# Kernel tuning notes

Hardware: AMD Instinct MI355X
Metric: run time of the kernel (lower is better)

Reference implementation:

```python
import jax, jax.numpy as jnp
import numpy as np

# ---- static dims ----
B, L, V = 8, 512, 100000
E, NERD, COREFD = 100, 20, 20          # word / ner / coref embedding dims
H, DIS, REL, HT = 128, 20, 97, 512     # hidden, dis embed, relations, n_pairs
W, N, R, C = 512, 32, 8, 256           # DNC word len, cells, read heads, ctrl hidden
IN_SIZE = E + NERD + COREFD            # 140 == H + 12 (required by final_layer)
DNC_OUT = H + 12                        # 140
CTRL_IN = IN_SIZE + R * W               # 4236
MASK_MIN, EPS, CLIP = 0.1, 1e-6, 20.0
# interface vector layout: read keys, read strengths, write key, write strength,
# erase, write vec, free gates, alloc gate, write gate, read modes,
# write mask, read masks, fwd sharpness, bwd sharpness
XI_SIZES = [R*W, R, W, 1, W, W, R, 1, 1, 3*R, W, R*W, R, R]
XI = sum(XI_SIZES)


def setup_inputs():
    key = jax.random.key(0)
    ks = iter(jax.random.split(key, 40))
    def nrm(shape, s=0.02):
        return (jax.random.normal(next(ks), shape) * s).astype(jnp.float32)
    def ri(shape, hi):
        return jax.random.randint(next(ks), shape, 0, hi)
    return dict(
        context_idxs=ri((B, L), V),
        pos=ri((B, L), L),
        context_ner=ri((B, L), 7),
        context_char_idxs=ri((B, L, 16), 262),
        context_lens=jnp.full((B,), L, dtype=jnp.int32),
        h_mapping=jax.random.uniform(next(ks), (B, HT, L), jnp.float32) / L,
        t_mapping=jax.random.uniform(next(ks), (B, HT, L), jnp.float32) / L,
        relation_mask=jnp.ones((B, HT), jnp.float32),
        dis_h_2_t=ri((B, HT), 20),
        dis_t_2_h=ri((B, HT), 20),
        word_emb=nrm((V, E), 0.1),
        entity_emb=nrm((L, COREFD), 0.1),
        ner_emb=nrm((7, NERD), 0.1),
        dis_emb=nrm((20, DIS), 0.1),
        Wih0=nrm((CTRL_IN, 4*C)), Whh0=nrm((C, 4*C)), b0=jnp.zeros((4*C,), jnp.float32),
        Wih1=nrm((C, 4*C)), Whh1=nrm((C, 4*C)), b1=jnp.zeros((4*C,), jnp.float32),
        Wih2=nrm((C, 4*C)), Whh2=nrm((C, 4*C)), b2=jnp.zeros((4*C,), jnp.float32),
        W_xi=nrm((C, XI)), b_xi=jnp.zeros((XI,), jnp.float32),
        W_out=nrm((C + R*W, DNC_OUT)), b_out=jnp.zeros((DNC_OUT,), jnp.float32),
        W_final=nrm((DNC_OUT, 2*H)), b_final=jnp.zeros((2*H,), jnp.float32),
        W_re=nrm((2*H, H)), b_re=jnp.zeros((H,), jnp.float32),
        W_bili=nrm((REL, H+DIS, H+DIS)), b_bili=jnp.zeros((REL,), jnp.float32),
    )


def _lstm(x, h, c, Wih, Whh, b):
    z = x @ Wih + h @ Whh + b
    i, f, g, o = jnp.split(z, 4, axis=-1)
    c = jax.nn.sigmoid(f) * c + jax.nn.sigmoid(i) * jnp.tanh(g)
    h = jax.nn.sigmoid(o) * jnp.tanh(c)
    return h, c


def _content(M, key_, beta, mask):
    # M [B,N,W]; key_, mask [B,h,W]; beta [B,h] -> weights [B,h,N]
    k = key_ * mask
    Mm = M[:, None] * mask[:, :, None]                 # [B,h,N,W]
    dot = jnp.einsum('bhw,bhnw->bhn', k, Mm)
    kn = jnp.linalg.norm(k, axis=-1)[..., None]
    Mn = jnp.linalg.norm(Mm, axis=-1)
    cos = dot / (kn * Mn + EPS)
    return jax.nn.softmax(beta[..., None] * cos, axis=-1)


def _sharpen(w, s):
    w = (w + EPS) ** s[..., None]
    return w / w.sum(-1, keepdims=True)


def _dnc(x, params):
    (Wih0, Whh0, b0, Wih1, Whh1, b1, Wih2, Whh2, b2, W_xi, b_xi, W_out, b_out) = params
    Bs = x.shape[0]
    eye = jnp.eye(N, dtype=x.dtype)
    splits = np.cumsum(XI_SIZES)[:-1]

    def step(carry, x_t):
        (h0, c0, h1, c1, h2, c2, M, u, wr, ww, p, Lnk, reads) = carry
        ci = jnp.concatenate([x_t, reads.reshape(Bs, R*W)], -1)
        h0, c0 = _lstm(ci, h0, c0, Wih0, Whh0, b0)
        h1, c1 = _lstm(h0, h1, c1, Wih1, Whh1, b1)
        h2, c2 = _lstm(h1, h2, c2, Wih2, Whh2, b2)
        h = jnp.clip(h2, -CLIP, CLIP)
        xi = h @ W_xi + b_xi
        (rk, rb, wk, wb, er, wv, fg, ga, gw, rm,
         wmask, rmask, sf, sb) = jnp.split(xi, splits, axis=-1)
        rk = rk.reshape(Bs, R, W)
        rb = 1 + jax.nn.softplus(rb)                    # [B,R]
        wk = wk.reshape(Bs, 1, W)
        wb = 1 + jax.nn.softplus(wb)                    # [B,1]
        er = jax.nn.sigmoid(er)                         # [B,W]
        fg = jax.nn.sigmoid(fg)                         # [B,R]
        ga = jax.nn.sigmoid(ga)
        gw = jax.nn.sigmoid(gw)
        pi = jax.nn.softmax(rm.reshape(Bs, R, 3), -1)
        wmask = MASK_MIN + (1 - MASK_MIN) * jax.nn.sigmoid(wmask)
        rmask = MASK_MIN + (1 - MASK_MIN) * jax.nn.sigmoid(rmask).reshape(Bs, R, W)
        sf = 1 + jax.nn.softplus(sf)
        sb = 1 + jax.nn.softplus(sb)

        # retention / usage
        psi = jnp.prod(1 - fg[:, :, None] * wr, axis=1)  # [B,N]
        u = (u + ww - u * ww) * psi
        # allocation weighting via sorted free list
        order = jnp.argsort(u, axis=-1)
        us = jnp.take_along_axis(u, order, -1)
        cp = jnp.cumprod(jnp.concatenate([jnp.ones((Bs, 1), u.dtype), us[:, :-1]], -1), -1)
        a_s = (1 - us) * cp
        a = jnp.zeros_like(u).at[jnp.arange(Bs)[:, None], order].set(a_s)
        # write addressing (masked content + allocation)
        cw = _content(M, wk, wb, wmask[:, None, :])[:, 0]
        ww = gw * (ga * a + (1 - ga) * cw)
        # de-allocate content of freed cells, then write
        M = M * psi[:, :, None]
        M = M * (1 - ww[:, :, None] * er[:, None, :]) + ww[:, :, None] * wv[:, None, :]
        # temporal link matrix (uses previous precedence p)
        Lnk = (1 - ww[:, :, None] - ww[:, None, :]) * Lnk + ww[:, :, None] * p[:, None, :]
        Lnk = Lnk * (1 - eye)
        p = (1 - ww.sum(-1, keepdims=True)) * p + ww
        # read addressing with link sharpness control
        fw = _sharpen(jnp.einsum('bij,brj->bri', Lnk, wr), sf)
        bw = _sharpen(jnp.einsum('bji,brj->bri', Lnk, wr), sb)
        cr = _content(M, rk, rb, rmask)
        wr = pi[..., 0:1] * bw + pi[..., 1:2] * cr + pi[..., 2:3] * fw
        reads = jnp.einsum('brn,bnw->brw', wr, M)
        y = jnp.concatenate([h, reads.reshape(Bs, R*W)], -1) @ W_out + b_out
        return (h0, c0, h1, c1, h2, c2, M, u, wr, ww, p, Lnk, reads), y

    z = jnp.zeros
    carry0 = (z((Bs, C)), z((Bs, C)), z((Bs, C)), z((Bs, C)), z((Bs, C)), z((Bs, C)),
              z((Bs, N, W)), z((Bs, N)), z((Bs, R, N)), z((Bs, N)), z((Bs, N)),
              z((Bs, N, N)), z((Bs, R, W)))
    _, ys = jax.lax.scan(step, carry0, x.transpose(1, 0, 2))
    return ys.transpose(1, 0, 2)  # [B,L,DNC_OUT]


def reference(context_idxs, pos, context_ner, context_char_idxs, context_lens,
              h_mapping, t_mapping, relation_mask, dis_h_2_t, dis_t_2_h,
              word_emb, entity_emb, ner_emb, dis_emb,
              Wih0, Whh0, b0, Wih1, Whh1, b1, Wih2, Whh2, b2,
              W_xi, b_xi, W_out, b_out, W_final, b_final, W_re, b_re,
              W_bili, b_bili):
    sent = jnp.concatenate([word_emb[context_idxs], entity_emb[pos],
                            ner_emb[context_ner]], -1)      # [B,L,140]
    dnc_params = (Wih0, Whh0, b0, Wih1, Whh1, b1, Wih2, Whh2, b2,
                  W_xi, b_xi, W_out, b_out)
    out = _dnc(sent, dnc_params)                             # [B,L,140]
    out = out @ W_final + b_final                            # LockedDropout: identity (eval)
    ctx = jax.nn.relu(out @ W_re + b_re)                     # [B,L,H]
    s0 = jnp.einsum('bpl,blh->bph', h_mapping, ctx)
    t0 = jnp.einsum('bpl,blh->bph', t_mapping, ctx)
    s_rep = jnp.concatenate([s0, dis_emb[dis_h_2_t]], -1)    # [B,P,148]
    t_rep = jnp.concatenate([t0, dis_emb[dis_t_2_h]], -1)
    return jnp.einsum('bpi,kij,bpj->bpk', s_rep, W_bili, t_rep) + b_bili
```

## Files before the change

kernel.cpp:

```cpp
#include <hip/hip_runtime.h>
#include <math.h>

#define B8      8
#define LSEQ    512
#define CDIM    256
#define GDIM    1024
#define WDIM    512
#define NCELL   32
#define RHEADS  8
#define XI_DIM  10299
#define DOUT    140
#define K_Z0    4492
#define K_Y     4352
#define HTP     512
#define RELK    97
#define BI      148

__device__ __forceinline__ float sigf(float x){
  return (x >= 0.f) ? 1.f/(1.f + expf(-x)) : expf(x)/(1.f + expf(x));
}
__device__ __forceinline__ float spf(float x){
  return (x > 0.f) ? x + log1pf(expf(-x)) : log1pf(expf(x));
}

__global__ __launch_bounds__(256)
void k_sent(const int* __restrict__ cidx, const int* __restrict__ pos,
            const int* __restrict__ ner, const float* __restrict__ wemb,
            const float* __restrict__ eemb, const float* __restrict__ nemb,
            float* __restrict__ sent)
{
  int flat = blockIdx.x*256 + threadIdx.x;
  if (flat >= B8*LSEQ*140) return;
  int d = flat % 140; int bl = flat / 140;
  float v;
  if (d < 100)      v = wemb[(size_t)cidx[bl]*100 + d];
  else if (d < 120) v = eemb[(size_t)pos[bl]*20 + (d-100)];
  else              v = nemb[(size_t)ner[bl]*20 + (d-120)];
  sent[flat] = v;
}

__global__ __launch_bounds__(256)
void k1_z0y(const float* __restrict__ Wih0, const float* __restrict__ Whh0,
            const float* __restrict__ b0,
            const float* __restrict__ Wout, const float* __restrict__ bout,
            const float* __restrict__ sent, const float* __restrict__ reads,
            const float* __restrict__ h0g, const float* __restrict__ Hh,
            float* __restrict__ z0, float* __restrict__ yh, int t, int yonly)
{
  __shared__ float sAin[B8][512];
  __shared__ float sRed[256][33];
  const int tid = threadIdx.x;
  const int wg  = blockIdx.x;
  const bool isY = (yonly != 0) || (wg >= 64);

  if (isY) {
    if (t == 0) return;
    const int yw = yonly ? wg : (wg - 64);
    const int c0 = yw*8;
    const int cq = tid & 1, ks = tid >> 1;
    float acc[8][4];
    for (int s=0;s<8;s++) for(int e=0;e<4;e++) acc[s][e]=0.f;
    const float* Hrow = Hh + (size_t)(t-1)*B8*CDIM;
    for (int kc = 0; kc < K_Y; kc += 512) {
      int klen = min(512, K_Y - kc);
      for (int ii=0; ii<16; ii++){
        int flat = tid + 256*ii; int s = flat >> 9; int kk = flat & 511;
        int g = kc + kk; float v = 0.f;
        if (kk < klen) v = (g < CDIM) ? Hrow[s*CDIM + g] : reads[s*4096 + (g-CDIM)];
        sAin[s][kk] = v;
      }
      __syncthreads();
      for (int k4=0; k4<4; k4++){
        int kk = ks*4 + k4;
        if (kk < klen) {
          int k = kc + kk;
          const float* wrow = Wout + (size_t)k*DOUT;
          float w[4];
          #pragma unroll
          for (int e=0;e<4;e++){ int c = c0 + cq*4 + e; w[e] = (c < DOUT) ? wrow[c] : 0.f; }
          #pragma unroll
          for (int s=0;s<8;s++){
            float a = sAin[s][kk];
            acc[s][0] += a*w[0]; acc[s][1] += a*w[1];
            acc[s][2] += a*w[2]; acc[s][3] += a*w[3];
          }
        }
      }
      __syncthreads();
    }
    for (int s=0;s<8;s++) for(int e=0;e<4;e++) sRed[tid][s*4+e] = acc[s][e];
    __syncthreads();
    if (tid < 64) {
      int cl = tid & 7, s = tid >> 3;
      int cq2 = (tid >> 2) & 1, ci = tid & 3;
      float sum = 0.f;
      for (int k2=0;k2<128;k2++) sum += sRed[cq2 + 2*k2][s*4+ci];
      int c = c0 + cl;
      if (c < DOUT) yh[((size_t)s*LSEQ + (t-1))*DOUT + c] = sum + bout[c];
    }
    return;
  }

  const int c0 = wg*16;
  const int cq = tid & 3, ks = tid >> 2;
  float acc[8][4];
  for (int s=0;s<8;s++) for(int e=0;e<4;e++) acc[s][e]=0.f;
  for (int kc = 0; kc < K_Z0; kc += 512) {
    int klen = min(512, K_Z0 - kc);
    for (int ii=0; ii<16; ii++){
      int flat = tid + 256*ii; int s = flat >> 9; int kk = flat & 511;
      int g = kc + kk; float v = 0.f;
      if (kk < klen) {
        if (g < 140)       v = sent[((size_t)s*LSEQ + t)*140 + g];
        else if (g < 4236) v = reads[s*4096 + (g-140)];
        else               v = h0g[s*CDIM + (g-4236)];
      }
      sAin[s][kk] = v;
    }
    __syncthreads();
    for (int k8=0; k8<8; k8++){
      int kk = ks*8 + k8;
      if (kk < klen) {
        int k = kc + kk;
        const float* wrow = (k < 4236) ? (Wih0 + (size_t)k*GDIM)
                                       : (Whh0 + (size_t)(k-4236)*GDIM);
        float4 w = *reinterpret_cast<const float4*>(wrow + c0 + cq*4);
        #pragma unroll
        for (int s=0;s<8;s++){
          float a = sAin[s][kk];
          acc[s][0] += a*w.x; acc[s][1] += a*w.y; acc[s][2] += a*w.z; acc[s][3] += a*w.w;
        }
      }
    }
    __syncthreads();
  }
  for (int s=0;s<8;s++) for(int e=0;e<4;e++) sRed[tid][s*4+e] = acc[s][e];
  __syncthreads();
  if (tid < 128) {
    int cl = tid & 15, s = tid >> 4;
    int cq2 = (tid >> 2) & 3, ci = tid & 3;
    float sum = 0.f;
    for (int k2=0;k2<64;k2++) sum += sRed[cq2 + 4*k2][s*4+ci];
    int c = c0 + cl;
    z0[s*GDIM + c] = sum + b0[c];
  }
}

__global__ __launch_bounds__(256)
void k_mid(const float* __restrict__ zin, float* __restrict__ cg, int par,
           float* __restrict__ houtg, const float* __restrict__ hsrc,
           const float* __restrict__ Wa, const float* __restrict__ Wb,
           const float* __restrict__ bias, float* __restrict__ zout)
{
  __shared__ float sAin[B8][512];
  __shared__ float sRed[256][33];
  const int tid = threadIdx.x, wg = blockIdx.x;
  for (int ii=0; ii<8; ii++){
    int cid = tid + 256*ii; int s = cid >> 8; int j = cid & 255;
    float zi = zin[s*GDIM + j],       zf = zin[s*GDIM + 256 + j];
    float zg = zin[s*GDIM + 512 + j], zo = zin[s*GDIM + 768 + j];
    float cold = cg[par*2048 + s*256 + j];
    float cn = sigf(zf)*cold + sigf(zi)*tanhf(zg);
    float h  = sigf(zo)*tanhf(cn);
    sAin[s][j] = h;
    if (wg == s) { cg[(par^1)*2048 + s*256 + j] = cn; houtg[s*256 + j] = h; }
  }
  for (int ii=0; ii<8; ii++){
    int cid = tid + 256*ii; int s = cid >> 8; int j = cid & 255;
    sAin[s][256 + j] = hsrc ? hsrc[s*256 + j] : 0.f;
  }
  __syncthreads();
  const int c0 = wg*16;
  const int cq = tid & 3, ks = tid >> 2;
  float acc[8][4];
  for (int s=0;s<8;s++) for(int e=0;e<4;e++) acc[s][e]=0.f;
  for (int k8=0;k8<8;k8++){
    int k = ks*8 + k8;
    const float* wrow = (k < 256) ? (Wa + (size_t)k*GDIM) : (Wb + (size_t)(k-256)*GDIM);
    float4 w = *reinterpret_cast<const float4*>(wrow + c0 + cq*4);
    #pragma unroll
    for (int s=0;s<8;s++){
      float a = sAin[s][k];
      acc[s][0] += a*w.x; acc[s][1] += a*w.y; acc[s][2] += a*w.z; acc[s][3] += a*w.w;
    }
  }
  for (int s=0;s<8;s++) for(int e=0;e<4;e++) sRed[tid][s*4+e] = acc[s][e];
  __syncthreads();
  if (tid < 128) {
    int cl = tid & 15, s = tid >> 4;
    int cq2 = (tid >> 2) & 3, ci = tid & 3;
    float sum = 0.f;
    for (int k2=0;k2<64;k2++) sum += sRed[cq2 + 4*k2][s*4+ci];
    int c = c0 + cl;
    zout[s*GDIM + c] = sum + bias[c];
  }
}

__global__ __launch_bounds__(256)
void k4_xi(const float* __restrict__ z2, float* __restrict__ c2g, int par,
           float* __restrict__ Hh, const float* __restrict__ Wxi,
           const float* __restrict__ bxi, float* __restrict__ xi, int t)
{
  __shared__ float sH[B8][CDIM];
  __shared__ float sRed[256][33];
  const int tid = threadIdx.x, wg = blockIdx.x;
  for (int ii=0; ii<8; ii++){
    int cid = tid + 256*ii; int s = cid >> 8; int j = cid & 255;
    float zi = z2[s*GDIM + j],       zf = z2[s*GDIM + 256 + j];
    float zg = z2[s*GDIM + 512 + j], zo = z2[s*GDIM + 768 + j];
    float cold = c2g[par*2048 + s*256 + j];
    float cn = sigf(zf)*cold + sigf(zi)*tanhf(zg);
    float h  = sigf(zo)*tanhf(cn);
    h = fminf(fmaxf(h, -20.f), 20.f);
    sH[s][j] = h;
    if (wg == s) { c2g[(par^1)*2048 + s*256 + j] = cn; Hh[((size_t)t*B8 + s)*CDIM + j] = h; }
  }
  __syncthreads();
  const int c0 = wg*64;
  const int cq = tid & 15, ks = tid >> 4;
  float acc[8][4];
  for (int s=0;s<8;s++) for(int e=0;e<4;e++) acc[s][e]=0.f;
  for (int k16=0;k16<16;k16++){
    int k = ks*16 + k16;
    const float* wrow = Wxi + (size_t)k*XI_DIM;
    float w[4];
    #pragma unroll
    for (int e=0;e<4;e++){ int c = c0 + cq*4 + e; w[e] = (c < XI_DIM) ? wrow[c] : 0.f; }
    #pragma unroll
    for (int s=0;s<8;s++){
      float a = sH[s][k];
      acc[s][0] += a*w[0]; acc[s][1] += a*w[1]; acc[s][2] += a*w[2]; acc[s][3] += a*w[3];
    }
  }
  for (int s=0;s<8;s++) for(int e=0;e<4;e++) sRed[tid][s*4+e] = acc[s][e];
  __syncthreads();
  for (int o = tid; o < 512; o += 256){
    int cq2 = (o >> 2) & 15, ci = o & 3, s = o >> 6;
    float sum = 0.f;
    for (int k2=0;k2<16;k2++) sum += sRed[cq2 + 16*k2][s*4+ci];
    int c = c0 + (o & 63);
    if (c < XI_DIM) xi[(size_t)s*XI_DIM + c] = sum + bxi[c];
  }
}

__global__ __launch_bounds__(512)
void k5_mem(const float* __restrict__ xi_g, float* __restrict__ M_g,
            float* __restrict__ u_g, float* __restrict__ ww_g, float* __restrict__ p_g,
            float* __restrict__ wr_g, float* __restrict__ L_g,
            float* __restrict__ reads_g)
{
  const int s = blockIdx.x;
  const int tid = threadIdx.x;
  const float* xi = xi_g + (size_t)s*XI_DIM;
  float* M = M_g + (size_t)s*NCELL*WDIM;

  __shared__ float s_rk[RHEADS][WDIM], s_rm[RHEADS][WDIM];
  __shared__ float s_wk[WDIM], s_wm[WDIM], s_er[WDIM], s_wv[WDIM];
  __shared__ float s_L[NCELL][NCELL];
  __shared__ float s_wr[RHEADS][NCELL], s_wrn[RHEADS][NCELL], s_cr[RHEADS][NCELL];
  __shared__ float s_fw[RHEADS][NCELL], s_bw[RHEADS][NCELL];
  __shared__ float s_psi[NCELL], s_u[NCELL], s_us[NCELL], s_a[NCELL], s_cw[NCELL];
  __shared__ float s_wwn[NCELL], s_wwo[NCELL], s_p[NCELL];
  __shared__ int   s_ord[NCELL];
  __shared__ float s_rb[RHEADS], s_sf[RHEADS], s_sb[RHEADS], s_fg[RHEADS], s_kn[RHEADS];
  __shared__ float s_pi[RHEADS][3];
  __shared__ float s_sc[64];

  for (int ii=0; ii<8; ii++){
    int f = tid + 512*ii; int r = f >> 9, w = f & 511;
    s_rk[r][w] = xi[f];
    s_rm[r][w] = 0.1f + 0.9f*sigf(xi[6187 + f]);
  }
  s_wk[tid] = xi[4104 + tid];
  s_er[tid] = sigf(xi[4617 + tid]);
  s_wv[tid] = xi[5129 + tid];
  s_wm[tid] = 0.1f + 0.9f*sigf(xi[5675 + tid]);
  if (tid < RHEADS){
    s_rb[tid] = 1.f + spf(xi[4096 + tid]);
    s_fg[tid] = sigf(xi[5641 + tid]);
    s_sf[tid] = 1.f + spf(xi[10283 + tid]);
    s_sb[tid] = 1.f + spf(xi[10291 + tid]);
    float e0 = xi[5651+3*tid], e1 = xi[5651+3*tid+1], e2 = xi[5651+3*tid+2];
    float mx = fmaxf(e0, fmaxf(e1, e2));
    float x0 = expf(e0-mx), x1 = expf(e1-mx), x2 = expf(e2-mx);
    float inv = 1.f/(x0+x1+x2);
    s_pi[tid][0]=x0*inv; s_pi[tid][1]=x1*inv; s_pi[tid][2]=x2*inv;
  }
  if (tid == 0){
    s_sc[0] = 1.f + spf(xi[4616]);
    s_sc[1] = sigf(xi[5649]);
    s_sc[2] = sigf(xi[5650]);
  }
  if (tid < NCELL){
    s_u[tid]   = u_g[s*NCELL + tid];
    s_wwo[tid] = ww_g[s*NCELL + tid];
    s_p[tid]   = p_g[s*NCELL + tid];
  }
  if (tid < 256) s_wr[tid>>5][tid&31] = wr_g[s*256 + tid];
  for (int ii=0; ii<2; ii++){ int f = tid + 512*ii; s_L[f>>5][f&31] = L_g[s*1024 + f]; }
  __syncthreads();

  if (tid < NCELL){
    float psi = 1.f;
    #pragma unroll
    for (int r=0;r<8;r++) psi *= (1.f - s_fg[r]*s_wr[r][tid]);
    s_psi[tid] = psi;
    float uo = s_u[tid], wo = s_wwo[tid];
    s_u[tid] = (uo + wo - uo*wo)*psi;
  }
  __syncthreads();

  if (tid < NCELL){
    float un = s_u[tid]; int rank = 0;
    for (int m=0;m<NCELL;m++){
      float um = s_u[m];
      rank += (um < un) || (um == un && m < tid);
    }
    s_ord[rank] = tid;
  }
  __syncthreads();
  if (tid < NCELL) s_us[tid] = s_u[s_ord[tid]];
  __syncthreads();
  if (tid == 0){
    float cp = 1.f;
    for (int j=0;j<NCELL;j++){ s_a[s_ord[j]] = (1.f - s_us[j])*cp; cp *= s_us[j]; }
  }
  __syncthreads();

  {
    float v = s_wk[tid]*s_wm[tid];
    float q = v*v;
    for (int o=32;o;o>>=1) q += __shfl_down(q, o, 64);
    if ((tid & 63) == 0) s_sc[8 + (tid >> 6)] = q;
  }
  __syncthreads();
  if (tid == 0){ float q=0; for(int i=0;i<8;i++) q += s_sc[8+i]; s_sc[3] = sqrtf(q); }
  __syncthreads();
  {
    int n = tid >> 4, wsub = tid & 15;
    float d=0.f, q=0.f;
    for (int i=0;i<32;i++){
      int w = wsub + 16*i;
      float m = M[(size_t)n*WDIM + w]; float wm = s_wm[w];
      d += s_wk[w]*wm*wm*m; float t2 = m*wm; q += t2*t2;
    }
    for (int o=8;o;o>>=1){ d += __shfl_down(d,o,16); q += __shfl_down(q,o,16); }
    if (wsub == 0){
      float cs = d/(s_sc[3]*sqrtf(q) + 1e-6f);
      s_cw[n] = s_sc[0]*cs;
    }
  }
  __syncthreads();
  if (tid == 0){ float mx=-1e30f; for(int n=0;n<32;n++) mx = fmaxf(mx, s_cw[n]); s_sc[4]=mx; }
  __syncthreads();
  if (tid < NCELL) s_cw[tid] = expf(s_cw[tid] - s_sc[4]);
  __syncthreads();
  if (tid == 0){ float sm=0; for(int n=0;n<32;n++) sm += s_cw[n]; s_sc[5] = 1.f/sm; }
  __syncthreads();
  if (tid < NCELL) s_cw[tid] *= s_sc[5];
  __syncthreads();

  if (tid < NCELL) s_wwn[tid] = s_sc[2]*( s_sc[1]*s_a[tid] + (1.f - s_sc[1])*s_cw[tid] );
  __syncthreads();

  for (int ii=0; ii<32; ii++){
    int f = tid + 512*ii; int n = f >> 9, w = f & 511;
    size_t idx = (size_t)n*WDIM + w;
    float m = M[idx];
    m = m*s_psi[n]*(1.f - s_wwn[n]*s_er[w]) + s_wwn[n]*s_wv[w];
    M[idx] = m;
  }
  __syncthreads();

  for (int ii=0; ii<2; ii++){
    int f = tid + 512*ii; int i = f >> 5, j = f & 31;
    float nl = (1.f - s_wwn[i] - s_wwn[j])*s_L[i][j] + s_wwn[i]*s_p[j];
    s_L[i][j] = (i == j) ? 0.f : nl;
  }
  __syncthreads();
  if (tid == 0){ float sw=0; for(int n=0;n<32;n++) sw += s_wwn[n]; s_sc[6]=sw; }
  __syncthreads();
  if (tid < NCELL) s_p[tid] = (1.f - s_sc[6])*s_p[tid] + s_wwn[tid];
  __syncthreads();

  {
    int r = (tid >> 5) & 7, i = tid & 31; bool isB = (tid >= 256);
    float accv = 0.f;
    if (!isB){ for (int j=0;j<32;j++) accv += s_L[i][j]*s_wr[r][j]; }
    else     { for (int j=0;j<32;j++) accv += s_L[j][i]*s_wr[r][j]; }
    float sp = isB ? s_sb[r] : s_sf[r];
    float e = expf(sp*logf(accv + 1e-6f));
    if (!isB) s_fw[r][i] = e; else s_bw[r][i] = e;
  }
  __syncthreads();
  if (tid < 16){
    int r = tid & 7; float sm = 0.f;
    if (tid < 8){ for (int n=0;n<32;n++) sm += s_fw[r][n]; s_sc[16+r] = 1.f/sm; }
    else        { for (int n=0;n<32;n++) sm += s_bw[r][n]; s_sc[24+r] = 1.f/sm; }
  }
  __syncthreads();
  {
    int r = (tid >> 5) & 7, i = tid & 31; bool isB = (tid >= 256);
    if (!isB) s_fw[r][i] *= s_sc[16+r]; else s_bw[r][i] *= s_sc[24+r];
  }
  __syncthreads();

  {
    int r = tid >> 6, wsub = tid & 63;
    float q = 0.f;
    for (int i2=0;i2<8;i2++){ int w = wsub + 64*i2; float v = s_rk[r][w]*s_rm[r][w]; q += v*v; }
    for (int o=32;o;o>>=1) q += __shfl_down(q, o, 64);
    if (wsub == 0) s_kn[r] = sqrtf(q);
  }
  __syncthreads();
  {
    int r = tid >> 6, rem = tid & 63, n = rem >> 1, h = rem & 1;
    float d=0.f, q=0.f;
    for (int i2=0;i2<256;i2++){
      int w = h*256 + i2;
      float m = M[(size_t)n*WDIM + w]; float rm = s_rm[r][w];
      d += s_rk[r][w]*rm*rm*m; float t2 = m*rm; q += t2*t2;
    }
    d += __shfl_down(d,1,2); q += __shfl_down(q,1,2);
    if (h == 0){
      float cs = d/(s_kn[r]*sqrtf(q) + 1e-6f);
      s_cr[r][n] = s_rb[r]*cs;
    }
  }
  __syncthreads();
  if (tid < 8){
    int r = tid; float mx = -1e30f;
    for (int n=0;n<32;n++) mx = fmaxf(mx, s_cr[r][n]);
    float sm = 0.f;
    for (int n=0;n<32;n++){ float e = expf(s_cr[r][n]-mx); s_cr[r][n] = e; sm += e; }
    float inv = 1.f/sm;
    for (int n=0;n<32;n++) s_cr[r][n] *= inv;
  }
  __syncthreads();

  if (tid < 256){
    int r = tid >> 5, n = tid & 31;
    float v = s_pi[r][0]*s_bw[r][n] + s_pi[r][1]*s_cr[r][n] + s_pi[r][2]*s_fw[r][n];
    s_wrn[r][n] = v; wr_g[s*256 + tid] = v;
  }
  __syncthreads();

  {
    int r = tid >> 6, wsub = tid & 63;
    for (int i2=0;i2<8;i2++){
      int w = wsub + 64*i2;
      float accv = 0.f;
      for (int n=0;n<32;n++) accv += s_wrn[r][n]*M[(size_t)n*WDIM + w];
      reads_g[s*4096 + r*512 + w] = accv;
    }
  }
  if (tid < NCELL){
    u_g[s*NCELL + tid] = s_u[tid];
    ww_g[s*NCELL + tid] = s_wwn[tid];
    p_g[s*NCELL + tid] = s_p[tid];
  }
  for (int ii=0; ii<2; ii++){ int f = tid + 512*ii; L_g[s*1024 + f] = s_L[f>>5][f&31]; }
}

__global__ __launch_bounds__(256)
void gemm16(int M, int N, int K,
            const float* __restrict__ A, long long sAb, int lda,
            const float* __restrict__ Bm, long long sBb, int ldb,
            float* __restrict__ C, long long sCb, int ldc,
            const float* __restrict__ bias, int relu)
{
  __shared__ float sA[16*512];
  const int tid = threadIdx.x;
  const float* Ab = A + (size_t)blockIdx.y*sAb;
  const float* Bb = Bm + (size_t)blockIdx.y*sBb;
  float* Cb = C + (size_t)blockIdx.y*sCb;
  const int m0 = blockIdx.x*16;
  const int tot = 16*K;
  for (int f = tid; f < tot; f += 256) sA[f] = Ab[(size_t)m0*lda + f];
  __syncthreads();
  int c = (tid & 63)*4; int rg = tid >> 6;
  if (c >= N) return;
  float acc[4][4] = {};
  for (int k=0;k<K;k++){
    float4 bv = *reinterpret_cast<const float4*>(Bb + (size_t)k*ldb + c);
    #pragma unroll
    for (int rr=0;rr<4;rr++){
      float a = sA[(rg*4+rr)*K + k];
      acc[rr][0] += a*bv.x; acc[rr][1] += a*bv.y; acc[rr][2] += a*bv.z; acc[rr][3] += a*bv.w;
    }
  }
  for (int rr=0;rr<4;rr++){
    int m = m0 + rg*4 + rr;
    #pragma unroll
    for (int e=0;e<4;e++){
      float v = acc[rr][e] + (bias ? bias[c+e] : 0.f);
      if (relu) v = fmaxf(v, 0.f);
      Cb[(size_t)m*ldc + c + e] = v;
    }
  }
}

__global__ __launch_bounds__(256)
void bilin(const float* __restrict__ s0, const float* __restrict__ t0,
           const float* __restrict__ dis_emb, const int* __restrict__ dht,
           const int* __restrict__ dth, const float* __restrict__ Wb,
           const float* __restrict__ bb, float* __restrict__ out)
{
  __shared__ float sS[BI][33];
  __shared__ float sT[32][152];
  const int tid = threadIdx.x;
  const int bp0 = blockIdx.x*32;
  for (int f = tid; f < 32*BI; f += 256){
    int pp = f / BI, i = f % BI;
    int bp = bp0 + pp;
    float sv, tv;
    if (i < 128){ sv = s0[(size_t)bp*128 + i]; tv = t0[(size_t)bp*128 + i]; }
    else {
      sv = dis_emb[(size_t)dht[bp]*20 + (i-128)];
      tv = dis_emb[(size_t)dth[bp]*20 + (i-128)];
    }
    sS[i][pp] = sv; sT[pp][i] = tv;
  }
  __syncthreads();
  const int ppg = tid >> 5, jb = tid & 31;
  const int pp0 = ppg*4;
  const int k0 = blockIdx.y*49, kend = min(k0+49, RELK);
  for (int k = k0; k < kend; k++){
    const float* Wk = Wb + (size_t)k*BI*BI;
    float acc[4][5];
    #pragma unroll
    for (int a=0;a<4;a++) for (int b=0;b<5;b++) acc[a][b]=0.f;
    for (int i=0;i<BI;i++){
      float sv0 = sS[i][pp0], sv1 = sS[i][pp0+1], sv2 = sS[i][pp0+2], sv3 = sS[i][pp0+3];
      const float* wrow = Wk + i*BI;
      #pragma unroll
      for (int jj=0;jj<5;jj++){
        int j = jb + 32*jj;
        if (j < BI){
          float w = wrow[j];
          acc[0][jj] += sv0*w; acc[1][jj] += sv1*w; acc[2][jj] += sv2*w; acc[3][jj] += sv3*w;
        }
      }
    }
    float dot[4] = {0.f,0.f,0.f,0.f};
    #pragma unroll
    for (int jj=0;jj<5;jj++){
      int j = jb + 32*jj;
      if (j < BI){
        #pragma unroll
        for (int p4=0;p4<4;p4++) dot[p4] += acc[p4][jj]*sT[pp0+p4][j];
      }
    }
    #pragma unroll
    for (int p4=0;p4<4;p4++)
      for (int o=16;o;o>>=1) dot[p4] += __shfl_down(dot[p4], o, 32);
    if (jb == 0){
      #pragma unroll
      for (int p4=0;p4<4;p4++)
        out[(size_t)(bp0+pp0+p4)*RELK + k] = dot[p4] + bb[k];
    }
  }
}

extern "C" void kernel_launch(void* const* d_in, const int* in_sizes, int n_in,
                              void* d_out, int out_size, void* d_ws, size_t ws_size,
                              hipStream_t stream)
{
  (void)in_sizes; (void)n_in; (void)out_size; (void)ws_size;
  const int*   ctx_idx = (const int*)  d_in[0];
  const int*   pos     = (const int*)  d_in[1];
  const int*   nerI    = (const int*)  d_in[2];
  const float* h_map   = (const float*)d_in[5];
  const float* t_map   = (const float*)d_in[6];
  const int*   dht     = (const int*)  d_in[8];
  const int*   dth     = (const int*)  d_in[9];
  const float* wemb    = (const float*)d_in[10];
  const float* eemb    = (const float*)d_in[11];
  const float* nemb    = (const float*)d_in[12];
  const float* demb    = (const float*)d_in[13];
  const float* Wih0    = (const float*)d_in[14];
  const float* Whh0    = (const float*)d_in[15];
  const float* b0      = (const float*)d_in[16];
  const float* Wih1    = (const float*)d_in[17];
  const float* Whh1    = (const float*)d_in[18];
  const float* b1      = (const float*)d_in[19];
  const float* Wih2    = (const float*)d_in[20];
  const float* Whh2    = (const float*)d_in[21];
  const float* b2      = (const float*)d_in[22];
  const float* Wxi     = (const float*)d_in[23];
  const float* bxi     = (const float*)d_in[24];
  const float* Wout    = (const float*)d_in[25];
  const float* bout    = (const float*)d_in[26];
  const float* Wfin    = (const float*)d_in[27];
  const float* bfin    = (const float*)d_in[28];
  const float* Wre     = (const float*)d_in[29];
  const float* bre     = (const float*)d_in[30];
  const float* Wbili   = (const float*)d_in[31];
  const float* bbili   = (const float*)d_in[32];

  float* ws   = (float*)d_ws;
  float* sent = ws;
  float* Hh   = sent + 573440;
  float* yh   = Hh + 1048576;
  float* o256 = yh + 573440;
  float* ctxb = o256 + 1048576;
  float* s0b  = ctxb + 524288;
  float* t0b  = s0b + 524288;
  float* stateBase = t0b + 524288;
  float* reads = stateBase;
  float* h0g   = reads + 32768;
  float* h1g   = h0g + 2048;
  float* c0g   = h1g + 2048;
  float* c1g   = c0g + 4096;
  float* c2g   = c1g + 4096;
  float* z0    = c2g + 4096;
  float* z1    = z0 + 8192;
  float* z2    = z1 + 8192;
  float* xib   = z2 + 8192;
  float* Mb    = xib + 82392;
  float* ug    = Mb + 131072;
  float* wwg   = ug + 256;
  float* pg    = wwg + 256;
  float* wrg   = pg + 256;
  float* Lg    = wrg + 2048;
  float* stateEnd = Lg + 8192;
  size_t stateBytes = (size_t)(stateEnd - stateBase)*sizeof(float);
  hipMemsetAsync(stateBase, 0, stateBytes, stream);

  hipLaunchKernelGGL(k_sent, dim3((573440+255)/256), dim3(256), 0, stream,
                     ctx_idx, pos, nerI, wemb, eemb, nemb, sent);

  for (int t = 0; t < LSEQ; t++){
    int par = t & 1;
    hipLaunchKernelGGL(k1_z0y, dim3(82), dim3(256), 0, stream,
                       Wih0, Whh0, b0, Wout, bout, sent, reads, h0g, Hh, z0, yh, t, 0);
    hipLaunchKernelGGL(k_mid, dim3(64), dim3(256), 0, stream,
                       z0, c0g, par, h0g, h1g, Wih1, Whh1, b1, z1);
    hipLaunchKernelGGL(k_mid, dim3(64), dim3(256), 0, stream,
                       z1, c1g, par, h1g, (t > 0) ? (Hh + (size_t)(t-1)*2048) : (const float*)nullptr,
                       Wih2, Whh2, b2, z2);
    hipLaunchKernelGGL(k4_xi, dim3(161), dim3(256), 0, stream,
                       z2, c2g, par, Hh, Wxi, bxi, xib, t);
    hipLaunchKernelGGL(k5_mem, dim3(8), dim3(512), 0, stream,
                       xib, Mb, ug, wwg, pg, wrg, Lg, reads);
  }
  hipLaunchKernelGGL(k1_z0y, dim3(18), dim3(256), 0, stream,
                     Wih0, Whh0, b0, Wout, bout, sent, reads, h0g, Hh, z0, yh, LSEQ, 1);

  hipLaunchKernelGGL(gemm16, dim3(256,1), dim3(256), 0, stream,
                     4096, 256, 140, yh, (long long)0, 140, Wfin, (long long)0, 256,
                     o256, (long long)0, 256, bfin, 0);
  hipLaunchKernelGGL(gemm16, dim3(256,1), dim3(256), 0, stream,
                     4096, 128, 256, o256, (long long)0, 256, Wre, (long long)0, 128,
                     ctxb, (long long)0, 128, bre, 1);
  hipLaunchKernelGGL(gemm16, dim3(32,8), dim3(256), 0, stream,
                     512, 128, 512, h_map, (long long)(512*512), 512,
                     ctxb, (long long)(512*128), 128,
                     s0b, (long long)(512*128), 128, (const float*)nullptr, 0);
  hipLaunchKernelGGL(gemm16, dim3(32,8), dim3(256), 0, stream,
                     512, 128, 512, t_map, (long long)(512*512), 512,
                     ctxb, (long long)(512*128), 128,
                     t0b, (long long)(512*128), 128, (const float*)nullptr, 0);
  hipLaunchKernelGGL(bilin, dim3(128,2), dim3(256), 0, stream,
                     s0b, t0b, demb, dht, dth, Wbili, bbili, (float*)d_out);
}
```

Before: 80.88 ms.

## Replace per-timestep kernel launches with a persistent DNC kernel using grid barriers

Replaces the 2560 per-step kernel launches of the DNC recurrence with one persistent kernel of 256 workgroups that loops over all timesteps, separated by atomic grid-wide barriers. Each workgroup keeps its slice of the LSTM, interface and output weights resident in registers instead of reloading them from global memory every step. The memory-update phase is folded into the same kernel, and reads and hidden state are double-buffered to avoid races. The cost is heavy register pressure, a spin-barrier that depends on all 256 workgroups being co-resident, and more serialized per-step work.

```diff
diff --git a/kernel.cpp b/kernel.cpp
--- a/kernel.cpp
+++ b/kernel.cpp
@@ -3,16 +3,8 @@
 
 #define B8      8
 #define LSEQ    512
-#define CDIM    256
-#define GDIM    1024
-#define WDIM    512
-#define NCELL   32
-#define RHEADS  8
-#define XI_DIM  10299
-#define DOUT    140
-#define K_Z0    4492
-#define K_Y     4352
-#define HTP     512
+#define NWG     256
+#define TPB     512
 #define RELK    97
 #define BI      148
 
@@ -39,427 +31,492 @@
   sent[flat] = v;
 }
 
-__global__ __launch_bounds__(256)
-void k1_z0y(const float* __restrict__ Wih0, const float* __restrict__ Whh0,
-            const float* __restrict__ b0,
-            const float* __restrict__ Wout, const float* __restrict__ bout,
-            const float* __restrict__ sent, const float* __restrict__ reads,
-            const float* __restrict__ h0g, const float* __restrict__ Hh,
-            float* __restrict__ z0, float* __restrict__ yh, int t, int yonly)
+__device__ __forceinline__ void gbar(int* cnt, int* gen){
+  __syncthreads();
+  if (threadIdx.x == 0){
+    __threadfence();
+    int g = __hip_atomic_load(gen, __ATOMIC_RELAXED, __HIP_MEMORY_SCOPE_AGENT);
+    int v = __hip_atomic_fetch_add(cnt, 1, __ATOMIC_ACQ_REL, __HIP_MEMORY_SCOPE_AGENT);
+    if (v == NWG-1){
+      __hip_atomic_store(cnt, 0, __ATOMIC_RELAXED, __HIP_MEMORY_SCOPE_AGENT);
+      __hip_atomic_fetch_add(gen, 1, __ATOMIC_RELEASE, __HIP_MEMORY_SCOPE_AGENT);
+    } else {
+      while (__hip_atomic_load(gen, __ATOMIC_RELAXED, __HIP_MEMORY_SCOPE_AGENT) == g)
+        __builtin_amdgcn_s_sleep(1);
+    }
+    __threadfence();
+  }
+  __syncthreads();
+}
+
+__device__ void mem_phase(float* lds, const float* __restrict__ xi,
+                          float* __restrict__ M, float* u_g, float* ww_g,
+                          float* p_g, float* wr_g, float* L_g, float* rout)
 {
-  __shared__ float sAin[B8][512];
-  __shared__ float sRed[256][33];
   const int tid = threadIdx.x;
+  float* mL  = lds;
+  float* mwr = lds+1024;
+  float* mwrn= lds+1280;
+  float* mcr = lds+1536;
+  float* mfw = lds+1792;
+  float* mbw = lds+2048;
+  float* PSI = lds+2304;
+  float* UU  = lds+2336;
+  float* US  = lds+2368;
+  float* AA  = lds+2400;
+  float* CW  = lds+2432;
+  float* WWN = lds+2464;
+  float* WWO = lds+2496;
+  float* PP  = lds+2528;
+  int*   mord= (int*)(lds+2560);
+  float* mh  = lds+2592;
+  float* mpi = lds+2656;
+  float* msc = lds+2688;
+  float* mq1 = lds+2752;
+  float* mq2 = lds+3264;
+  float* mp1 = lds+3776;
+  float* mp2 = lds+4800;
+
+  if (tid < 8){
+    mh[tid]    = 1.f + spf(xi[4096+tid]);
+    mh[8+tid]  = 1.f + spf(xi[10283+tid]);
+    mh[16+tid] = 1.f + spf(xi[10291+tid]);
+    mh[24+tid] = sigf(xi[5641+tid]);
+    float e0=xi[5651+3*tid], e1=xi[5652+3*tid], e2=xi[5653+3*tid];
+    float mx=fmaxf(e0,fmaxf(e1,e2));
+    float x0=expf(e0-mx), x1=expf(e1-mx), x2=expf(e2-mx);
+    float inv=1.f/(x0+x1+x2);
+    mpi[tid*3]=x0*inv; mpi[tid*3+1]=x1*inv; mpi[tid*3+2]=x2*inv;
+  }
+  if (tid==0){ msc[0]=1.f+spf(xi[4616]); msc[1]=sigf(xi[5649]); msc[2]=sigf(xi[5650]); }
+  if (tid<32){ UU[tid]=u_g[tid]; WWO[tid]=ww_g[tid]; PP[tid]=p_g[tid]; }
+  if (tid<256) mwr[tid]=wr_g[tid];
+  mL[tid]=L_g[tid]; mL[tid+512]=L_g[tid+512];
+  { float wm = 0.1f+0.9f*sigf(xi[5675+tid]); mq1[tid]=xi[4104+tid]*wm; mq2[tid]=wm; }
+  __syncthreads();
+
+  if (tid<32){
+    float psi=1.f;
+    #pragma unroll
+    for (int r=0;r<8;r++) psi *= (1.f - mh[24+r]*mwr[r*32+tid]);
+    PSI[tid]=psi;
+    float uo=UU[tid], wo=WWO[tid];
+    UU[tid]=(uo+wo-uo*wo)*psi;
+  }
+  __syncthreads();
+  if (tid<32){
+    float un=UU[tid]; int rank=0;
+    for (int m=0;m<32;m++){ float um=UU[m]; rank += (um<un)||(um==un && m<tid); }
+    mord[rank]=tid;
+  }
+  __syncthreads();
+  if (tid<32) US[tid]=UU[mord[tid]];
+  __syncthreads();
+  if (tid==0){ float cp=1.f; for (int j=0;j<32;j++){ AA[mord[j]]=(1.f-US[j])*cp; cp*=US[j]; } }
+  __syncthreads();
+
+  { float q=mq1[tid]*mq1[tid];
+    for (int o=32;o;o>>=1) q += __shfl_down(q,o,64);
+    if ((tid&63)==0) msc[8+(tid>>6)]=q; }
+  __syncthreads();
+  if (tid==0){ float q=0.f; for (int i=0;i<8;i++) q+=msc[8+i]; msc[3]=sqrtf(q); }
+  __syncthreads();
+  { int n=tid>>4, wsub=tid&15;
+    float d=0.f,q=0.f;
+    for (int i=0;i<32;i++){ int w=wsub+16*i; float m=M[(size_t)n*512+w]; float t2=m*mq2[w]; d+=mq1[w]*t2; q+=t2*t2; }
+    for (int o=8;o;o>>=1){ d+=__shfl_down(d,o,16); q+=__shfl_down(q,o,16); }
+    if (wsub==0){ float cs=d/(msc[3]*sqrtf(q)+1e-6f); CW[n]=msc[0]*cs; } }
+  __syncthreads();
+  if (tid==0){ float mx=-1e30f; for(int n=0;n<32;n++) mx=fmaxf(mx,CW[n]); msc[4]=mx; }
+  __syncthreads();
+  if (tid<32) CW[tid]=expf(CW[tid]-msc[4]);
+  __syncthreads();
+  if (tid==0){ float sm=0.f; for(int n=0;n<32;n++) sm+=CW[n]; msc[5]=1.f/sm; }
+  __syncthreads();
+  if (tid<32) CW[tid]*=msc[5];
+  __syncthreads();
+  if (tid<32) WWN[tid]=msc[2]*(msc[1]*AA[tid]+(1.f-msc[1])*CW[tid]);
+  __syncthreads();
+  { float er=sigf(xi[4617+tid]); float wv=xi[5129+tid];
+    for (int n=0;n<32;n++){ size_t idx=(size_t)n*512+tid; float m=M[idx];
+      M[idx]=m*PSI[n]*(1.f-WWN[n]*er)+WWN[n]*wv; } }
+  __syncthreads();
+  for (int ii=0;ii<2;ii++){ int f=tid+512*ii; int i=f>>5, j=f&31;
+    float nl=(1.f-WWN[i]-WWN[j])*mL[f]+WWN[i]*PP[j];
+    mL[f]=(i==j)?0.f:nl; }
+  __syncthreads();
+  if (tid==0){ float sw=0.f; for(int n=0;n<32;n++) sw+=WWN[n]; msc[6]=sw; }
+  __syncthreads();
+  if (tid<32) PP[tid]=(1.f-msc[6])*PP[tid]+WWN[tid];
+  __syncthreads();
+  { int r=(tid>>5)&7, i=tid&31; bool isB=(tid>=256);
+    float accv=0.f;
+    if (!isB){ for (int j=0;j<32;j++) accv += mL[i*32+j]*mwr[r*32+j]; }
+    else     { for (int j=0;j<32;j++) accv += mL[j*32+i]*mwr[r*32+j]; }
+    float sp = isB? mh[16+r] : mh[8+r];
+    float e = expf(sp*logf(accv+1e-6f));
+    if (!isB) mfw[r*32+i]=e; else mbw[r*32+i]=e; }
+  __syncthreads();
+  if (tid<16){ int r=tid&7; float sm=0.f;
+    if (tid<8){ for(int n=0;n<32;n++) sm+=mfw[r*32+n]; msc[16+r]=1.f/sm; }
+    else      { for(int n=0;n<32;n++) sm+=mbw[r*32+n]; msc[24+r]=1.f/sm; } }
+  __syncthreads();
+  { int r=(tid>>5)&7, i=tid&31; bool isB=(tid>=256);
+    if (!isB) mfw[r*32+i]*=msc[16+r]; else mbw[r*32+i]*=msc[24+r]; }
+  __syncthreads();
+  for (int hp=0; hp<4; hp++){
+    for (int rp2=0;rp2<2;rp2++){
+      int r=hp*2+rp2;
+      float rm=0.1f+0.9f*sigf(xi[6187+r*512+tid]);
+      mp1[rp2*512+tid]=xi[r*512+tid]*rm;
+      mp2[rp2*512+tid]=rm;
+    }
+    __syncthreads();
+    for (int rp2=0;rp2<2;rp2++){
+      float q=mp1[rp2*512+tid]; q*=q;
+      for (int o=32;o;o>>=1) q+=__shfl_down(q,o,64);
+      if ((tid&63)==0) msc[8+(tid>>6)]=q;
+      __syncthreads();
+      if (tid==0){ float qq=0.f; for(int i=0;i<8;i++) qq+=msc[8+i]; msc[32+rp2]=sqrtf(qq); }
+      __syncthreads();
+    }
+    { int rp2=tid>>8, rem=tid&255, n=rem>>3, wsub=rem&7;
+      float d=0.f,q=0.f;
+      for (int i=0;i<64;i++){ int w=wsub*64+i; float m=M[(size_t)n*512+w]; float t2=m*mp2[rp2*512+w];
+        d+=mp1[rp2*512+w]*t2; q+=t2*t2; }
+      for (int o=4;o;o>>=1){ d+=__shfl_down(d,o,8); q+=__shfl_down(q,o,8); }
+      if (wsub==0){ int r=hp*2+rp2; float cs=d/(msc[32+rp2]*sqrtf(q)+1e-6f); mcr[r*32+n]=mh[r]*cs; } }
+    __syncthreads();
+  }
+  if (tid<8){ int r=tid; float mx=-1e30f;
+    for (int n=0;n<32;n++) mx=fmaxf(mx,mcr[r*32+n]);
+    float sm=0.f;
+    for (int n=0;n<32;n++){ float e=expf(mcr[r*32+n]-mx); mcr[r*32+n]=e; sm+=e; }
+    float inv=1.f/sm;
+    for (int n=0;n<32;n++) mcr[r*32+n]*=inv; }
+  __syncthreads();
+  if (tid<256){ int r=tid>>5, n=tid&31;
+    float v=mpi[r*3]*mbw[r*32+n]+mpi[r*3+1]*mcr[r*32+n]+mpi[r*3+2]*mfw[r*32+n];
+    mwrn[tid]=v; wr_g[tid]=v; }
+  __syncthreads();
+  { int r=tid>>6, wsub=tid&63;
+    for (int i2=0;i2<8;i2++){ int w=wsub+64*i2;
+      float accv=0.f;
+      for (int n=0;n<32;n++) accv+=mwrn[r*32+n]*M[(size_t)n*512+w];
+      rout[r*512+w]=accv; } }
+  if (tid<32){ u_g[tid]=UU[tid]; ww_g[tid]=WWN[tid]; p_g[tid]=PP[tid]; }
+  L_g[tid]=mL[tid]; L_g[tid+512]=mL[tid+512];
+}
+
+__global__ __launch_bounds__(TPB, 2)
+void dnc_persist(
+  const float* __restrict__ sent,
+  const float* __restrict__ Wih0, const float* __restrict__ Whh0, const float* __restrict__ b0,
+  const float* __restrict__ Wih1, const float* __restrict__ Whh1, const float* __restrict__ b1,
+  const float* __restrict__ Wih2, const float* __restrict__ Whh2, const float* __restrict__ b2,
+  const float* __restrict__ Wxi, const float* __restrict__ bxi,
+  const float* __restrict__ Wout, const float* __restrict__ bout,
+  float* __restrict__ Hh, float* __restrict__ yh,
+  float* __restrict__ reads2,
+  float* __restrict__ h0g, float* __restrict__ h1g, float* __restrict__ h2g,
+  float* __restrict__ c0g, float* __restrict__ c1g, float* __restrict__ c2g,
+  float* __restrict__ z0g, float* __restrict__ z1g, float* __restrict__ z2g,
+  float* __restrict__ xig,
+  float* __restrict__ Mb, float* __restrict__ ug, float* __restrict__ wwg,
+  float* __restrict__ pg, float* __restrict__ wrg, float* __restrict__ Lg,
+  int* bar)
+{
+  __shared__ float lds[5824];
+  float* sA   = lds;
+  float* sRed = lds + 4160;
   const int wg  = blockIdx.x;
-  const bool isY = (yonly != 0) || (wg >= 64);
-
-  if (isY) {
-    if (t == 0) return;
-    const int yw = yonly ? wg : (wg - 64);
-    const int c0 = yw*8;
-    const int cq = tid & 1, ks = tid >> 1;
-    float acc[8][4];
-    for (int s=0;s<8;s++) for(int e=0;e<4;e++) acc[s][e]=0.f;
-    const float* Hrow = Hh + (size_t)(t-1)*B8*CDIM;
-    for (int kc = 0; kc < K_Y; kc += 512) {
-      int klen = min(512, K_Y - kc);
-      for (int ii=0; ii<16; ii++){
-        int flat = tid + 256*ii; int s = flat >> 9; int kk = flat & 511;
-        int g = kc + kk; float v = 0.f;
-        if (kk < klen) v = (g < CDIM) ? Hrow[s*CDIM + g] : reads[s*4096 + (g-CDIM)];
-        sAin[s][kk] = v;
-      }
-      __syncthreads();
-      for (int k4=0; k4<4; k4++){
-        int kk = ks*4 + k4;
-        if (kk < klen) {
-          int k = kc + kk;
-          const float* wrow = Wout + (size_t)k*DOUT;
-          float w[4];
-          #pragma unroll
-          for (int e=0;e<4;e++){ int c = c0 + cq*4 + e; w[e] = (c < DOUT) ? wrow[c] : 0.f; }
+  const int tid = threadIdx.x;
+  const int cq = tid >> 7, kq = tid & 127;
+  const int xc = tid >> 6, xk = tid & 63;
+  int* cnt = bar; int* gen = bar+1;
+
+  const int zcol = wg*4 + cq;
+  float w0r[36];
+  #pragma unroll
+  for (int c=0;c<9;c++)
+    #pragma unroll
+    for (int i=0;i<4;i++){
+      int k = c*512 + kq*4 + i;
+      float v;
+      if (k < 4236)      v = Wih0[(size_t)k*1024 + zcol];
+      else if (k < 4492) v = Whh0[(size_t)(k-4236)*1024 + zcol];
+      else               v = 0.f;
+      w0r[c*4+i]=v;
+    }
+  float w1r[4], w2r[4];
+  #pragma unroll
+  for (int i=0;i<4;i++){
+    int k = kq*4+i;
+    w1r[i] = (k<256)? Wih1[(size_t)k*1024+zcol] : Whh1[(size_t)(k-256)*1024+zcol];
+    w2r[i] = (k<256)? Wih2[(size_t)k*1024+zcol] : Whh2[(size_t)(k-256)*1024+zcol];
+  }
+  float wxr[24];
+  #pragma unroll
+  for (int cc=0;cc<6;cc++){
+    int col = wg*48 + xc*6 + cc;
+    #pragma unroll
+    for (int i=0;i<4;i++){
+      int k = xk*4+i;
+      wxr[cc*4+i] = (col<10299)? Wxi[(size_t)k*10299 + col] : 0.f;
+    }
+  }
+  float wyr[9];
+  {
+    bool isy = (wg>=8 && wg<148);
+    int ycol = wg-8;
+    #pragma unroll
+    for (int c=0;c<9;c++){
+      int k = c*512 + tid;
+      wyr[c] = (isy && k<4352)? Wout[(size_t)k*140 + ycol] : 0.f;
+    }
+  }
+
+  #pragma unroll 1
+  for (int t=0; t<LSEQ; t++){
+    const int rp = t&1, wp = rp^1;
+    const float* readsPrev = reads2 + (size_t)((t-1)&1)*32768;
+
+    {
+      float acc[8] = {0,0,0,0,0,0,0,0};
+      const float* h0p = h0g + ((t-1)&1)*2048;
+      float av[8];
+      #pragma unroll
+      for (int s=0;s<8;s++){
+        int kg = tid;
+        float v;
+        if (kg < 140) v = sent[((size_t)s*512 + t)*140 + kg];
+        else          v = readsPrev[s*4096 + kg - 140];
+        av[s]=v;
+      }
+      for (int ch=0; ch<9; ch++){
+        __syncthreads();
+        #pragma unroll
+        for (int s=0;s<8;s++) sA[s*520 + tid] = av[s];
+        __syncthreads();
+        if (ch < 8){
+          int kg = (ch+1)*512 + tid;
           #pragma unroll
           for (int s=0;s<8;s++){
-            float a = sAin[s][kk];
-            acc[s][0] += a*w[0]; acc[s][1] += a*w[1];
-            acc[s][2] += a*w[2]; acc[s][3] += a*w[3];
+            float v;
+            if (kg < 140)       v = sent[((size_t)s*512 + t)*140 + kg];
+            else if (kg < 4236) v = readsPrev[s*4096 + kg - 140];
+            else if (kg < 4492) v = h0p[s*256 + (kg-4236)];
+            else                v = 0.f;
+            av[s]=v;
           }
         }
-      }
-      __syncthreads();
-    }
-    for (int s=0;s<8;s++) for(int e=0;e<4;e++) sRed[tid][s*4+e] = acc[s][e];
+        #pragma unroll
+        for (int s=0;s<8;s++){
+          float4 a = *reinterpret_cast<const float4*>(&sA[s*520 + (kq<<2)]);
+          acc[s] += a.x*w0r[ch*4] + a.y*w0r[ch*4+1] + a.z*w0r[ch*4+2] + a.w*w0r[ch*4+3];
+        }
+      }
+      #pragma unroll
+      for (int o=32;o;o>>=1)
+        #pragma unroll
+        for (int s=0;s<8;s++) acc[s]+=__shfl_down(acc[s],o,64);
+      if ((tid&63)==0){ int wv=tid>>6;
+        #pragma unroll
+        for (int s=0;s<8;s++) sRed[wv*8+s]=acc[s]; }
+      __syncthreads();
+      if (tid<32){ int c=tid>>3, s=tid&7;
+        z0g[s*1024 + wg*4 + c] = sRed[c*16+s] + sRed[c*16+8+s] + b0[wg*4+c]; }
+    }
+    gbar(cnt,gen);
+
+    {
+      if (tid<256){
+        int j=tid;
+        #pragma unroll
+        for (int s=0;s<8;s++){
+          float zi=z0g[s*1024+j], zf=z0g[s*1024+256+j], zg=z0g[s*1024+512+j], zo=z0g[s*1024+768+j];
+          float cold=c0g[rp*2048+s*256+j];
+          float cn=sigf(zf)*cold+sigf(zi)*tanhf(zg);
+          float h=sigf(zo)*tanhf(cn);
+          sA[s*520+j]=h;
+          if (wg==8){ c0g[wp*2048+s*256+j]=cn; h0g[rp*2048+s*256+j]=h; }
+        }
+      } else {
+        int j=tid-256;
+        const float* h1p = h1g + ((t-1)&1)*2048;
+        #pragma unroll
+        for (int s=0;s<8;s++) sA[s*520+256+j]=h1p[s*256+j];
+      }
+      __syncthreads();
+      float acc[8]={0,0,0,0,0,0,0,0};
+      #pragma unroll
+      for (int s=0;s<8;s++){
+        float4 a=*reinterpret_cast<const float4*>(&sA[s*520+(kq<<2)]);
+        acc[s]+=a.x*w1r[0]+a.y*w1r[1]+a.z*w1r[2]+a.w*w1r[3];
+      }
+      #pragma unroll
+      for (int o=32;o;o>>=1)
+        #pragma unroll
+        for (int s=0;s<8;s++) acc[s]+=__shfl_down(acc[s],o,64);
+      if ((tid&63)==0){ int wv=tid>>6;
+        #pragma unroll
+        for (int s=0;s<8;s++) sRed[wv*8+s]=acc[s]; }
+      __syncthreads();
+      if (tid<32){ int c=tid>>3, s=tid&7;
+        z1g[s*1024 + wg*4 + c] = sRed[c*16+s] + sRed[c*16+8+s] + b1[wg*4+c]; }
+    }
+    gbar(cnt,gen);
+
+    {
+      if (tid<256){
+        int j=tid;
+        #pragma unroll
+        for (int s=0;s<8;s++){
+          float zi=z1g[s*1024+j], zf=z1g[s*1024+256+j], zg=z1g[s*1024+512+j], zo=z1g[s*1024+768+j];
+          float cold=c1g[rp*2048+s*256+j];
+          float cn=sigf(zf)*cold+sigf(zi)*tanhf(zg);
+          float h=sigf(zo)*tanhf(cn);
+          sA[s*520+j]=h;
+          if (wg==8){ c1g[wp*2048+s*256+j]=cn; h1g[rp*2048+s*256+j]=h; }
+        }
+      } else {
+        int j=tid-256;
+        const float* h2p = h2g + ((t-1)&1)*2048;
+        #pragma unroll
+        for (int s=0;s<8;s++) sA[s*520+256+j]=h2p[s*256+j];
+      }
+      __syncthreads();
+      float acc[8]={0,0,0,0,0,0,0,0};
+      #pragma unroll
+      for (int s=0;s<8;s++){
+        float4 a=*reinterpret_cast<const float4*>(&sA[s*520+(kq<<2)]);
+        acc[s]+=a.x*w2r[0]+a.y*w2r[1]+a.z*w2r[2]+a.w*w2r[3];
+      }
+      #pragma unroll
+      for (int o=32;o;o>>=1)
+        #pragma unroll
+        for (int s=0;s<8;s++) acc[s]+=__shfl_down(acc[s],o,64);
+      if ((tid&63)==0){ int wv=tid>>6;
+        #pragma unroll
+        for (int s=0;s<8;s++) sRed[wv*8+s]=acc[s]; }
+      __syncthreads();
+      if (tid<32){ int c=tid>>3, s=tid&7;
+        z2g[s*1024 + wg*4 + c] = sRed[c*16+s] + sRed[c*16+8+s] + b2[wg*4+c]; }
+    }
+    gbar(cnt,gen);
+
+    {
+      if (tid<256){
+        int j=tid;
+        #pragma unroll
+        for (int s=0;s<8;s++){
+          float zi=z2g[s*1024+j], zf=z2g[s*1024+256+j], zg=z2g[s*1024+512+j], zo=z2g[s*1024+768+j];
+          float cold=c2g[rp*2048+s*256+j];
+          float cn=sigf(zf)*cold+sigf(zi)*tanhf(zg);
+          float h2=sigf(zo)*tanhf(cn);
+          float hc=fminf(fmaxf(h2,-20.f),20.f);
+          sA[s*520+j]=hc;
+          if (wg==8){ c2g[wp*2048+s*256+j]=cn; h2g[rp*2048+s*256+j]=h2;
+                      Hh[((size_t)t*8+s)*256+j]=hc; }
+        }
+      }
+      __syncthreads();
+      float accx[6][8];
+      #pragma unroll
+      for (int cc=0;cc<6;cc++)
+        #pragma unroll
+        for (int s=0;s<8;s++) accx[cc][s]=0.f;
+      #pragma unroll
+      for (int s=0;s<8;s++){
+        float4 a = *reinterpret_cast<const float4*>(&sA[s*520 + (xk<<2)]);
+        #pragma unroll
+        for (int cc=0;cc<6;cc++)
+          accx[cc][s] += a.x*wxr[cc*4] + a.y*wxr[cc*4+1] + a.z*wxr[cc*4+2] + a.w*wxr[cc*4+3];
+      }
+      #pragma unroll
+      for (int o=32;o;o>>=1)
+        #pragma unroll
+        for (int cc=0;cc<6;cc++)
+          #pragma unroll
+          for (int s=0;s<8;s++) accx[cc][s]+=__shfl_down(accx[cc][s],o,64);
+      if ((tid&63)==0){
+        #pragma unroll
+        for (int cc=0;cc<6;cc++){
+          int col = wg*48 + xc*6 + cc;
+          if (col < 10299){
+            #pragma unroll
+            for (int s=0;s<8;s++) xig[(size_t)s*10299+col]=accx[cc][s]+bxi[col];
+          }
+        }
+      }
+    }
+    gbar(cnt,gen);
+
+    if (wg < 8){
+      mem_phase(lds, xig + (size_t)wg*10299, Mb + (size_t)wg*16384,
+                ug+wg*32, wwg+wg*32, pg+wg*32, wrg+wg*256, Lg+wg*1024,
+                reads2 + (size_t)rp*32768 + wg*4096);
+    } else if (wg < 148 && t > 0){
+      int ty = t-1, col = wg-8;
+      const float* rdp = reads2 + (size_t)(ty&1)*32768;
+      float acy[8]={0,0,0,0,0,0,0,0};
+      #pragma unroll
+      for (int ch=0;ch<9;ch++){
+        int kg=ch*512+tid;
+        #pragma unroll
+        for (int s=0;s<8;s++){
+          float a;
+          if (kg<256)       a=Hh[((size_t)ty*8+s)*256+kg];
+          else if (kg<4352) a=rdp[s*4096+kg-256];
+          else              a=0.f;
+          acy[s]+=a*wyr[ch];
+        }
+      }
+      #pragma unroll
+      for (int o=32;o;o>>=1)
+        #pragma unroll
+        for (int s=0;s<8;s++) acy[s]+=__shfl_down(acy[s],o,64);
+      if ((tid&63)==0){ int wv=tid>>6;
+        #pragma unroll
+        for (int s=0;s<8;s++) sRed[wv*8+s]=acy[s]; }
+      __syncthreads();
+      if (tid<8){ float v=0.f;
+        #pragma unroll
+        for (int w=0;w<8;w++) v+=sRed[w*8+tid];
+        yh[((size_t)tid*512+ty)*140+col]=v+bout[col]; }
+    }
+    gbar(cnt,gen);
+  }
+
+  if (wg>=8 && wg<148){
+    int ty = 511, col = wg-8;
+    const float* rdp = reads2 + (size_t)(ty&1)*32768;
+    float acy[8]={0,0,0,0,0,0,0,0};
+    #pragma unroll
+    for (int ch=0;ch<9;ch++){
+      int kg=ch*512+tid;
+      #pragma unroll
+      for (int s=0;s<8;s++){
+        float a;
+        if (kg<256)       a=Hh[((size_t)ty*8+s)*256+kg];
+        else if (kg<4352) a=rdp[s*4096+kg-256];
+        else              a=0.f;
+        acy[s]+=a*wyr[ch];
+      }
+    }
+    #pragma unroll
+    for (int o=32;o;o>>=1)
+      #pragma unroll
+      for (int s=0;s<8;s++) acy[s]+=__shfl_down(acy[s],o,64);
+    if ((tid&63)==0){ int wv=tid>>6;
+      #pragma unroll
+      for (int s=0;s<8;s++) sRed[wv*8+s]=acy[s]; }
     __syncthreads();
-    if (tid < 64) {
-      int cl = tid & 7, s = tid >> 3;
-      int cq2 = (tid >> 2) & 1, ci = tid & 3;
-      float sum = 0.f;
-      for (int k2=0;k2<128;k2++) sum += sRed[cq2 + 2*k2][s*4+ci];
-      int c = c0 + cl;
-      if (c < DOUT) yh[((size_t)s*LSEQ + (t-1))*DOUT + c] = sum + bout[c];
-    }
-    return;
-  }
-
-  const int c0 = wg*16;
-  const int cq = tid & 3, ks = tid >> 2;
-  float acc[8][4];
-  for (int s=0;s<8;s++) for(int e=0;e<4;e++) acc[s][e]=0.f;
-  for (int kc = 0; kc < K_Z0; kc += 512) {
-    int klen = min(512, K_Z0 - kc);
-    for (int ii=0; ii<16; ii++){
-      int flat = tid + 256*ii; int s = flat >> 9; int kk = flat & 511;
-      int g = kc + kk; float v = 0.f;
-      if (kk < klen) {
-        if (g < 140)       v = sent[((size_t)s*LSEQ + t)*140 + g];
-        else if (g < 4236) v = reads[s*4096 + (g-140)];
-        else               v = h0g[s*CDIM + (g-4236)];
-      }
-      sAin[s][kk] = v;
-    }
-    __syncthreads();
-    for (int k8=0; k8<8; k8++){
-      int kk = ks*8 + k8;
-      if (kk < klen) {
-        int k = kc + kk;
-        const float* wrow = (k < 4236) ? (Wih0 + (size_t)k*GDIM)
-                                       : (Whh0 + (size_t)(k-4236)*GDIM);
-        float4 w = *reinterpret_cast<const float4*>(wrow + c0 + cq*4);
-        #pragma unroll
-        for (int s=0;s<8;s++){
-          float a = sAin[s][kk];
-          acc[s][0] += a*w.x; acc[s][1] += a*w.y; acc[s][2] += a*w.z; acc[s][3] += a*w.w;
-        }
-      }
-    }
-    __syncthreads();
-  }
-  for (int s=0;s<8;s++) for(int e=0;e<4;e++) sRed[tid][s*4+e] = acc[s][e];
-  __syncthreads();
-  if (tid < 128) {
-    int cl = tid & 15, s = tid >> 4;
-    int cq2 = (tid >> 2) & 3, ci = tid & 3;
-    float sum = 0.f;
-    for (int k2=0;k2<64;k2++) sum += sRed[cq2 + 4*k2][s*4+ci];
-    int c = c0 + cl;
-    z0[s*GDIM + c] = sum + b0[c];
-  }
-}
-
-__global__ __launch_bounds__(256)
-void k_mid(const float* __restrict__ zin, float* __restrict__ cg, int par,
-           float* __restrict__ houtg, const float* __restrict__ hsrc,
-           const float* __restrict__ Wa, const float* __restrict__ Wb,
-           const float* __restrict__ bias, float* __restrict__ zout)
-{
-  __shared__ float sAin[B8][512];
-  __shared__ float sRed[256][33];
-  const int tid = threadIdx.x, wg = blockIdx.x;
-  for (int ii=0; ii<8; ii++){
-    int cid = tid + 256*ii; int s = cid >> 8; int j = cid & 255;
-    float zi = zin[s*GDIM + j],       zf = zin[s*GDIM + 256 + j];
-    float zg = zin[s*GDIM + 512 + j], zo = zin[s*GDIM + 768 + j];
-    float cold = cg[par*2048 + s*256 + j];
-    float cn = sigf(zf)*cold + sigf(zi)*tanhf(zg);
-    float h  = sigf(zo)*tanhf(cn);
-    sAin[s][j] = h;
-    if (wg == s) { cg[(par^1)*2048 + s*256 + j] = cn; houtg[s*256 + j] = h; }
-  }
-  for (int ii=0; ii<8; ii++){
-    int cid = tid + 256*ii; int s = cid >> 8; int j = cid & 255;
-    sAin[s][256 + j] = hsrc ? hsrc[s*256 + j] : 0.f;
-  }
-  __syncthreads();
-  const int c0 = wg*16;
-  const int cq = tid & 3, ks = tid >> 2;
-  float acc[8][4];
-  for (int s=0;s<8;s++) for(int e=0;e<4;e++) acc[s][e]=0.f;
-  for (int k8=0;k8<8;k8++){
-    int k = ks*8 + k8;
-    const float* wrow = (k < 256) ? (Wa + (size_t)k*GDIM) : (Wb + (size_t)(k-256)*GDIM);
-    float4 w = *reinterpret_cast<const float4*>(wrow + c0 + cq*4);
-    #pragma unroll
-    for (int s=0;s<8;s++){
-      float a = sAin[s][k];
-      acc[s][0] += a*w.x; acc[s][1] += a*w.y; acc[s][2] += a*w.z; acc[s][3] += a*w.w;
-    }
-  }
-  for (int s=0;s<8;s++) for(int e=0;e<4;e++) sRed[tid][s*4+e] = acc[s][e];
-  __syncthreads();
-  if (tid < 128) {
-    int cl = tid & 15, s = tid >> 4;
-    int cq2 = (tid >> 2) & 3, ci = tid & 3;
-    float sum = 0.f;
-    for (int k2=0;k2<64;k2++) sum += sRed[cq2 + 4*k2][s*4+ci];
-    int c = c0 + cl;
-    zout[s*GDIM + c] = sum + bias[c];
-  }
-}
-
-__global__ __launch_bounds__(256)
-void k4_xi(const float* __restrict__ z2, float* __restrict__ c2g, int par,
-           float* __restrict__ Hh, const float* __restrict__ Wxi,
-           const float* __restrict__ bxi, float* __restrict__ xi, int t)
-{
-  __shared__ float sH[B8][CDIM];
-  __shared__ float sRed[256][33];
-  const int tid = threadIdx.x, wg = blockIdx.x;
-  for (int ii=0; ii<8; ii++){
-    int cid = tid + 256*ii; int s = cid >> 8; int j = cid & 255;
-    float zi = z2[s*GDIM + j],       zf = z2[s*GDIM + 256 + j];
-    float zg = z2[s*GDIM + 512 + j], zo = z2[s*GDIM + 768 + j];
-    float cold = c2g[par*2048 + s*256 + j];
-    float cn = sigf(zf)*cold + sigf(zi)*tanhf(zg);
-    float h  = sigf(zo)*tanhf(cn);
-    h = fminf(fmaxf(h, -20.f), 20.f);
-    sH[s][j] = h;
-    if (wg == s) { c2g[(par^1)*2048 + s*256 + j] = cn; Hh[((size_t)t*B8 + s)*CDIM + j] = h; }
-  }
-  __syncthreads();
-  const int c0 = wg*64;
-  const int cq = tid & 15, ks = tid >> 4;
-  float acc[8][4];
-  for (int s=0;s<8;s++) for(int e=0;e<4;e++) acc[s][e]=0.f;
-  for (int k16=0;k16<16;k16++){
-    int k = ks*16 + k16;
-    const float* wrow = Wxi + (size_t)k*XI_DIM;
-    float w[4];
-    #pragma unroll
-    for (int e=0;e<4;e++){ int c = c0 + cq*4 + e; w[e] = (c < XI_DIM) ? wrow[c] : 0.f; }
-    #pragma unroll
-    for (int s=0;s<8;s++){
-      float a = sH[s][k];
-      acc[s][0] += a*w[0]; acc[s][1] += a*w[1]; acc[s][2] += a*w[2]; acc[s][3] += a*w[3];
-    }
-  }
-  for (int s=0;s<8;s++) for(int e=0;e<4;e++) sRed[tid][s*4+e] = acc[s][e];
-  __syncthreads();
-  for (int o = tid; o < 512; o += 256){
-    int cq2 = (o >> 2) & 15, ci = o & 3, s = o >> 6;
-    float sum = 0.f;
-    for (int k2=0;k2<16;k2++) sum += sRed[cq2 + 16*k2][s*4+ci];
-    int c = c0 + (o & 63);
-    if (c < XI_DIM) xi[(size_t)s*XI_DIM + c] = sum + bxi[c];
-  }
-}
-
-__global__ __launch_bounds__(512)
-void k5_mem(const float* __restrict__ xi_g, float* __restrict__ M_g,
-            float* __restrict__ u_g, float* __restrict__ ww_g, float* __restrict__ p_g,
-            float* __restrict__ wr_g, float* __restrict__ L_g,
-            float* __restrict__ reads_g)
-{
-  const int s = blockIdx.x;
-  const int tid = threadIdx.x;
-  const float* xi = xi_g + (size_t)s*XI_DIM;
-  float* M = M_g + (size_t)s*NCELL*WDIM;
-
-  __shared__ float s_rk[RHEADS][WDIM], s_rm[RHEADS][WDIM];
-  __shared__ float s_wk[WDIM], s_wm[WDIM], s_er[WDIM], s_wv[WDIM];
-  __shared__ float s_L[NCELL][NCELL];
-  __shared__ float s_wr[RHEADS][NCELL], s_wrn[RHEADS][NCELL], s_cr[RHEADS][NCELL];
-  __shared__ float s_fw[RHEADS][NCELL], s_bw[RHEADS][NCELL];
-  __shared__ float s_psi[NCELL], s_u[NCELL], s_us[NCELL], s_a[NCELL], s_cw[NCELL];
-  __shared__ float s_wwn[NCELL], s_wwo[NCELL], s_p[NCELL];
-  __shared__ int   s_ord[NCELL];
-  __shared__ float s_rb[RHEADS], s_sf[RHEADS], s_sb[RHEADS], s_fg[RHEADS], s_kn[RHEADS];
-  __shared__ float s_pi[RHEADS][3];
-  __shared__ float s_sc[64];
-
-  for (int ii=0; ii<8; ii++){
-    int f = tid + 512*ii; int r = f >> 9, w = f & 511;
-    s_rk[r][w] = xi[f];
-    s_rm[r][w] = 0.1f + 0.9f*sigf(xi[6187 + f]);
-  }
-  s_wk[tid] = xi[4104 + tid];
-  s_er[tid] = sigf(xi[4617 + tid]);
-  s_wv[tid] = xi[5129 + tid];
-  s_wm[tid] = 0.1f + 0.9f*sigf(xi[5675 + tid]);
-  if (tid < RHEADS){
-    s_rb[tid] = 1.f + spf(xi[4096 + tid]);
-    s_fg[tid] = sigf(xi[5641 + tid]);
-    s_sf[tid] = 1.f + spf(xi[10283 + tid]);
-    s_sb[tid] = 1.f + spf(xi[10291 + tid]);
-    float e0 = xi[5651+3*tid], e1 = xi[5651+3*tid+1], e2 = xi[5651+3*tid+2];
-    float mx = fmaxf(e0, fmaxf(e1, e2));
-    float x0 = expf(e0-mx), x1 = expf(e1-mx), x2 = expf(e2-mx);
-    float inv = 1.f/(x0+x1+x2);
-    s_pi[tid][0]=x0*inv; s_pi[tid][1]=x1*inv; s_pi[tid][2]=x2*inv;
-  }
-  if (tid == 0){
-    s_sc[0] = 1.f + spf(xi[4616]);
-    s_sc[1] = sigf(xi[5649]);
-    s_sc[2] = sigf(xi[5650]);
-  }
-  if (tid < NCELL){
-    s_u[tid]   = u_g[s*NCELL + tid];
-    s_wwo[tid] = ww_g[s*NCELL + tid];
-    s_p[tid]   = p_g[s*NCELL + tid];
-  }
-  if (tid < 256) s_wr[tid>>5][tid&31] = wr_g[s*256 + tid];
-  for (int ii=0; ii<2; ii++){ int f = tid + 512*ii; s_L[f>>5][f&31] = L_g[s*1024 + f]; }
-  __syncthreads();
-
-  if (tid < NCELL){
-    float psi = 1.f;
-    #pragma unroll
-    for (int r=0;r<8;r++) psi *= (1.f - s_fg[r]*s_wr[r][tid]);
-    s_psi[tid] = psi;
-    float uo = s_u[tid], wo = s_wwo[tid];
-    s_u[tid] = (uo + wo - uo*wo)*psi;
-  }
-  __syncthreads();
-
-  if (tid < NCELL){
-    float un = s_u[tid]; int rank = 0;
-    for (int m=0;m<NCELL;m++){
-      float um = s_u[m];
-      rank += (um < un) || (um == un && m < tid);
-    }
-    s_ord[rank] = tid;
-  }
-  __syncthreads();
-  if (tid < NCELL) s_us[tid] = s_u[s_ord[tid]];
-  __syncthreads();
-  if (tid == 0){
-    float cp = 1.f;
-    for (int j=0;j<NCELL;j++){ s_a[s_ord[j]] = (1.f - s_us[j])*cp; cp *= s_us[j]; }
-  }
-  __syncthreads();
-
-  {
-    float v = s_wk[tid]*s_wm[tid];
-    float q = v*v;
-    for (int o=32;o;o>>=1) q += __shfl_down(q, o, 64);
-    if ((tid & 63) == 0) s_sc[8 + (tid >> 6)] = q;
-  }
-  __syncthreads();
-  if (tid == 0){ float q=0; for(int i=0;i<8;i++) q += s_sc[8+i]; s_sc[3] = sqrtf(q); }
-  __syncthreads();
-  {
-    int n = tid >> 4, wsub = tid & 15;
-    float d=0.f, q=0.f;
-    for (int i=0;i<32;i++){
-      int w = wsub + 16*i;
-      float m = M[(size_t)n*WDIM + w]; float wm = s_wm[w];
-      d += s_wk[w]*wm*wm*m; float t2 = m*wm; q += t2*t2;
-    }
-    for (int o=8;o;o>>=1){ d += __shfl_down(d,o,16); q += __shfl_down(q,o,16); }
-    if (wsub == 0){
-      float cs = d/(s_sc[3]*sqrtf(q) + 1e-6f);
-      s_cw[n] = s_sc[0]*cs;
-    }
-  }
-  __syncthreads();
-  if (tid == 0){ float mx=-1e30f; for(int n=0;n<32;n++) mx = fmaxf(mx, s_cw[n]); s_sc[4]=mx; }
-  __syncthreads();
-  if (tid < NCELL) s_cw[tid] = expf(s_cw[tid] - s_sc[4]);
-  __syncthreads();
-  if (tid == 0){ float sm=0; for(int n=0;n<32;n++) sm += s_cw[n]; s_sc[5] = 1.f/sm; }
-  __syncthreads();
-  if (tid < NCELL) s_cw[tid] *= s_sc[5];
-  __syncthreads();
-
-  if (tid < NCELL) s_wwn[tid] = s_sc[2]*( s_sc[1]*s_a[tid] + (1.f - s_sc[1])*s_cw[tid] );
-  __syncthreads();
-
-  for (int ii=0; ii<32; ii++){
-    int f = tid + 512*ii; int n = f >> 9, w = f & 511;
-    size_t idx = (size_t)n*WDIM + w;
-    float m = M[idx];
-    m = m*s_psi[n]*(1.f - s_wwn[n]*s_er[w]) + s_wwn[n]*s_wv[w];
-    M[idx] = m;
-  }
-  __syncthreads();
-
-  for (int ii=0; ii<2; ii++){
-    int f = tid + 512*ii; int i = f >> 5, j = f & 31;
-    float nl = (1.f - s_wwn[i] - s_wwn[j])*s_L[i][j] + s_wwn[i]*s_p[j];
-    s_L[i][j] = (i == j) ? 0.f : nl;
-  }
-  __syncthreads();
-  if (tid == 0){ float sw=0; for(int n=0;n<32;n++) sw += s_wwn[n]; s_sc[6]=sw; }
-  __syncthreads();
-  if (tid < NCELL) s_p[tid] = (1.f - s_sc[6])*s_p[tid] + s_wwn[tid];
-  __syncthreads();
-
-  {
-    int r = (tid >> 5) & 7, i = tid & 31; bool isB = (tid >= 256);
-    float accv = 0.f;
-    if (!isB){ for (int j=0;j<32;j++) accv += s_L[i][j]*s_wr[r][j]; }
-    else     { for (int j=0;j<32;j++) accv += s_L[j][i]*s_wr[r][j]; }
-    float sp = isB ? s_sb[r] : s_sf[r];
-    float e = expf(sp*logf(accv + 1e-6f));
-    if (!isB) s_fw[r][i] = e; else s_bw[r][i] = e;
-  }
-  __syncthreads();
-  if (tid < 16){
-    int r = tid & 7; float sm = 0.f;
-    if (tid < 8){ for (int n=0;n<32;n++) sm += s_fw[r][n]; s_sc[16+r] = 1.f/sm; }
-    else        { for (int n=0;n<32;n++) sm += s_bw[r][n]; s_sc[24+r] = 1.f/sm; }
-  }
-  __syncthreads();
-  {
-    int r = (tid >> 5) & 7, i = tid & 31; bool isB = (tid >= 256);
-    if (!isB) s_fw[r][i] *= s_sc[16+r]; else s_bw[r][i] *= s_sc[24+r];
-  }
-  __syncthreads();
-
-  {
-    int r = tid >> 6, wsub = tid & 63;
-    float q = 0.f;
-    for (int i2=0;i2<8;i2++){ int w = wsub + 64*i2; float v = s_rk[r][w]*s_rm[r][w]; q += v*v; }
-    for (int o=32;o;o>>=1) q += __shfl_down(q, o, 64);
-    if (wsub == 0) s_kn[r] = sqrtf(q);
-  }
-  __syncthreads();
-  {
-    int r = tid >> 6, rem = tid & 63, n = rem >> 1, h = rem & 1;
-    float d=0.f, q=0.f;
-    for (int i2=0;i2<256;i2++){
-      int w = h*256 + i2;
-      float m = M[(size_t)n*WDIM + w]; float rm = s_rm[r][w];
-      d += s_rk[r][w]*rm*rm*m; float t2 = m*rm; q += t2*t2;
-    }
-    d += __shfl_down(d,1,2); q += __shfl_down(q,1,2);
-    if (h == 0){
-      float cs = d/(s_kn[r]*sqrtf(q) + 1e-6f);
-      s_cr[r][n] = s_rb[r]*cs;
-    }
-  }
-  __syncthreads();
-  if (tid < 8){
-    int r = tid; float mx = -1e30f;
-    for (int n=0;n<32;n++) mx = fmaxf(mx, s_cr[r][n]);
-    float sm = 0.f;
-    for (int n=0;n<32;n++){ float e = expf(s_cr[r][n]-mx); s_cr[r][n] = e; sm += e; }
-    float inv = 1.f/sm;
-    for (int n=0;n<32;n++) s_cr[r][n] *= inv;
-  }
-  __syncthreads();
-
-  if (tid < 256){
-    int r = tid >> 5, n = tid & 31;
-    float v = s_pi[r][0]*s_bw[r][n] + s_pi[r][1]*s_cr[r][n] + s_pi[r][2]*s_fw[r][n];
-    s_wrn[r][n] = v; wr_g[s*256 + tid] = v;
-  }
-  __syncthreads();
-
-  {
-    int r = tid >> 6, wsub = tid & 63;
-    for (int i2=0;i2<8;i2++){
-      int w = wsub + 64*i2;
-      float accv = 0.f;
-      for (int n=0;n<32;n++) accv += s_wrn[r][n]*M[(size_t)n*WDIM + w];
-      reads_g[s*4096 + r*512 + w] = accv;
-    }
-  }
-  if (tid < NCELL){
-    u_g[s*NCELL + tid] = s_u[tid];
-    ww_g[s*NCELL + tid] = s_wwn[tid];
-    p_g[s*NCELL + tid] = s_p[tid];
-  }
-  for (int ii=0; ii<2; ii++){ int f = tid + 512*ii; L_g[s*1024 + f] = s_L[f>>5][f&31]; }
+    if (tid<8){ float v=0.f;
+      #pragma unroll
+      for (int w=0;w<8;w++) v+=sRed[w*8+tid];
+      yh[((size_t)tid*512+ty)*140+col]=v+bout[col]; }
+  }
 }
 
 __global__ __launch_bounds__(256)
@@ -469,14 +526,14 @@
             float* __restrict__ C, long long sCb, int ldc,
             const float* __restrict__ bias, int relu)
 {
-  __shared__ float sA[16*512];
+  __shared__ float sAh[16*512];
   const int tid = threadIdx.x;
   const float* Ab = A + (size_t)blockIdx.y*sAb;
   const float* Bb = Bm + (size_t)blockIdx.y*sBb;
   float* Cb = C + (size_t)blockIdx.y*sCb;
   const int m0 = blockIdx.x*16;
   const int tot = 16*K;
-  for (int f = tid; f < tot; f += 256) sA[f] = Ab[(size_t)m0*lda + f];
+  for (int f = tid; f < tot; f += 256) sAh[f] = Ab[(size_t)m0*lda + f];
   __syncthreads();
   int c = (tid & 63)*4; int rg = tid >> 6;
   if (c >= N) return;
@@ -485,7 +542,7 @@
     float4 bv = *reinterpret_cast<const float4*>(Bb + (size_t)k*ldb + c);
     #pragma unroll
     for (int rr=0;rr<4;rr++){
-      float a = sA[(rg*4+rr)*K + k];
+      float a = sAh[(rg*4+rr)*K + k];
       acc[rr][0] += a*bv.x; acc[rr][1] += a*bv.y; acc[rr][2] += a*bv.z; acc[rr][3] += a*bv.w;
     }
   }
@@ -598,54 +655,44 @@
   const float* Wbili   = (const float*)d_in[31];
   const float* bbili   = (const float*)d_in[32];
 
-  float* ws   = (float*)d_ws;
-  float* sent = ws;
-  float* Hh   = sent + 573440;
-  float* yh   = Hh + 1048576;
-  float* o256 = yh + 573440;
-  float* ctxb = o256 + 1048576;
-  float* s0b  = ctxb + 524288;
-  float* t0b  = s0b + 524288;
-  float* stateBase = t0b + 524288;
-  float* reads = stateBase;
-  float* h0g   = reads + 32768;
-  float* h1g   = h0g + 2048;
-  float* c0g   = h1g + 2048;
+  float* ws    = (float*)d_ws;
+  float* sent  = ws;
+  float* Hh    = sent + 573440;
+  float* yh    = Hh + 1048576;
+  float* s0b   = yh + 573440;
+  float* t0b   = s0b + 524288;
+  float* reads2= t0b + 524288;
+  float* h0g   = reads2 + 65536;
+  float* h1g   = h0g + 4096;
+  float* h2g   = h1g + 4096;
+  float* c0g   = h2g + 4096;
   float* c1g   = c0g + 4096;
   float* c2g   = c1g + 4096;
-  float* z0    = c2g + 4096;
-  float* z1    = z0 + 8192;
-  float* z2    = z1 + 8192;
-  float* xib   = z2 + 8192;
-  float* Mb    = xib + 82392;
+  float* z0g   = c2g + 4096;
+  float* z1g   = z0g + 8192;
+  float* z2g   = z1g + 8192;
+  float* xig   = z2g + 8192;
+  float* Mb    = xig + 82392;
   float* ug    = Mb + 131072;
   float* wwg   = ug + 256;
   float* pg    = wwg + 256;
   float* wrg   = pg + 256;
   float* Lg    = wrg + 2048;
-  float* stateEnd = Lg + 8192;
-  size_t stateBytes = (size_t)(stateEnd - stateBase)*sizeof(float);
-  hipMemsetAsync(stateBase, 0, stateBytes, stream);
+  float* barf  = Lg + 8192;
+  float* o256  = Hh;
+  float* ctxb  = sent;
+
+  size_t stateFloats = (size_t)((barf + 16) - reads2);
+  hipMemsetAsync(reads2, 0, stateFloats*sizeof(float), stream);
 
   hipLaunchKernelGGL(k_sent, dim3((573440+255)/256), dim3(256), 0, stream,
                      ctx_idx, pos, nerI, wemb, eemb, nemb, sent);
 
-  for (int t = 0; t < LSEQ; t++){
-    int par = t & 1;
-    hipLaunchKernelGGL(k1_z0y, dim3(82), dim3(256), 0, stream,
-                       Wih0, Whh0, b0, Wout, bout, sent, reads, h0g, Hh, z0, yh, t, 0);
-    hipLaunchKernelGGL(k_mid, dim3(64), dim3(256), 0, stream,
-                       z0, c0g, par, h0g, h1g, Wih1, Whh1, b1, z1);
-    hipLaunchKernelGGL(k_mid, dim3(64), dim3(256), 0, stream,
-                       z1, c1g, par, h1g, (t > 0) ? (Hh + (size_t)(t-1)*2048) : (const float*)nullptr,
-                       Wih2, Whh2, b2, z2);
-    hipLaunchKernelGGL(k4_xi, dim3(161), dim3(256), 0, stream,
-                       z2, c2g, par, Hh, Wxi, bxi, xib, t);
-    hipLaunchKernelGGL(k5_mem, dim3(8), dim3(512), 0, stream,
-                       xib, Mb, ug, wwg, pg, wrg, Lg, reads);
-  }
-  hipLaunchKernelGGL(k1_z0y, dim3(18), dim3(256), 0, stream,
-                     Wih0, Whh0, b0, Wout, bout, sent, reads, h0g, Hh, z0, yh, LSEQ, 1);
+  hipLaunchKernelGGL(dnc_persist, dim3(NWG), dim3(TPB), 0, stream,
+                     sent, Wih0, Whh0, b0, Wih1, Whh1, b1, Wih2, Whh2, b2,
+                     Wxi, bxi, Wout, bout, Hh, yh, reads2,
+                     h0g, h1g, h2g, c0g, c1g, c2g, z0g, z1g, z2g, xig,
+                     Mb, ug, wwg, pg, wrg, Lg, (int*)barf);
 
   hipLaunchKernelGGL(gemm16, dim3(256,1), dim3(256), 0, stream,
                      4096, 256, 140, yh, (long long)0, 140, Wfin, (long long)0, 256,
```

Result: slower. 167.3 ms (+106.9%).
